# Optimization experiments

Hardware: AMD Instinct MI355X
Metric: run time of the kernel (lower is better)

The kernel has to match this reference:

```python
import jax, jax.numpy as jnp
from jax import lax
import numpy as np

B = 512
IN_CAPS, OUT_CAPS, IN_DIM, OUT_DIM, ITERS = 32 * 6 * 6, 10, 8, 16, 3
EPS = 1e-8


def setup_inputs() -> dict:
    key = jax.random.key(0)
    ks = jax.random.split(key, 12)
    inp = {
        "x": jax.random.normal(ks[0], (B, 1, 28, 28), dtype=jnp.float32),
        "conv1_w": jax.random.normal(ks[1], (256, 1, 9, 9), dtype=jnp.float32) * 0.05,
        "conv1_b": jnp.zeros((256,), dtype=jnp.float32),
        "conv2_w": jax.random.normal(ks[2], (256, 256, 9, 9), dtype=jnp.float32) * 0.02,
        "conv2_b": jnp.zeros((256,), dtype=jnp.float32),
        "W": jax.random.normal(ks[3], (IN_CAPS, OUT_CAPS, IN_DIM, OUT_DIM), dtype=jnp.float32) * 0.1,
        "d1_w": jax.random.normal(ks[4], (OUT_DIM * OUT_CAPS, 512), dtype=jnp.float32) * 0.05,
        "d1_b": jnp.zeros((512,), dtype=jnp.float32),
        "d2_w": jax.random.normal(ks[5], (512, 1024), dtype=jnp.float32) * 0.05,
        "d2_b": jnp.zeros((1024,), dtype=jnp.float32),
        "d3_w": jax.random.normal(ks[6], (1024, 28 * 28), dtype=jnp.float32) * 0.05,
        "d3_b": jnp.zeros((28 * 28,), dtype=jnp.float32),
    }
    return inp


def _squash(s):
    # s2/(1+s2) * s/sqrt(s2+eps), norm over last dim
    s2 = jnp.sum(s * s, axis=-1, keepdims=True)
    return s2 / (1.0 + s2) * (s / jnp.sqrt(s2 + EPS))


def _conv(x, w, b, stride):
    y = lax.conv_general_dilated(x, w, (stride, stride), "VALID",
                                 dimension_numbers=("NCHW", "OIHW", "NCHW"))
    return y + b[None, :, None, None]


def reference(x, conv1_w, conv1_b, conv2_w, conv2_b, W,
              d1_w, d1_b, d2_w, d2_b, d3_w, d3_b):
    h = jax.nn.relu(_conv(x, conv1_w, conv1_b, 1))          # [B,256,20,20]
    h = _conv(h, conv2_w, conv2_b, 2)                       # [B,256,6,6]
    u = h.reshape(h.shape[0], 8, IN_CAPS).transpose(0, 2, 1)  # [B,1152,8]
    u = _squash(u)

    # dynamic routing
    u_hat = jnp.einsum("ijnm,bin->bijm", W, u)              # [B,1152,10,16]
    b_log = jnp.zeros((u.shape[0], IN_CAPS, OUT_CAPS), dtype=u.dtype)
    v = None
    for _ in range(ITERS):
        c = jax.nn.softmax(b_log, axis=1)                   # over in_capsules (as original)
        s = jnp.einsum("bij,bijm->bjm", c, u_hat)           # [B,10,16]
        v = _squash(s)
        b_log = b_log + jnp.einsum("bjm,bijm->bij", v, u_hat)
    caps = v                                                # [B,10,16]

    pred = jnp.argmax(jnp.sum(caps * caps, axis=-1), axis=-1)  # [B]
    mask = jax.lax.stop_gradient(jax.nn.one_hot(pred, OUT_CAPS, dtype=caps.dtype))
    dec_in = (caps * mask[:, :, None]).reshape(caps.shape[0], -1)  # [B,160]
    r = jax.nn.relu(dec_in @ d1_w + d1_b)
    r = jax.nn.relu(r @ d2_w + d2_b)
    r = jax.nn.sigmoid(r @ d3_w + d3_b)
    recon = r.reshape(-1, 1, 28, 28)
    return caps, recon, pred
```

## Files before the change

kernel.cpp:

```cpp
#include <hip/hip_runtime.h>

#define CAPS_EPS 1e-8f

typedef __attribute__((ext_vector_type(8))) short short8;
typedef __attribute__((ext_vector_type(4))) float f32x4;

__device__ inline ushort bf16_rn(float f) {
    uint u = __float_as_uint(f);
    u += 0x7fff + ((u >> 16) & 1);
    return (ushort)(u >> 16);
}
__device__ inline float bf16_f(ushort h) { return __uint_as_float((uint)h << 16); }

__device__ __forceinline__ void gld16(const void* g, void* l) {
    __builtin_amdgcn_global_load_lds(
        (const __attribute__((address_space(1))) unsigned int*)g,
        (__attribute__((address_space(3))) unsigned int*)l, 16, 0, 0);
}


__global__ __launch_bounds__(256) void k_wt2(const float* __restrict__ w2,
                                             ushort* __restrict__ wBhi,
                                             ushort* __restrict__ wBlo) {
    int n = blockIdx.x;
    int c = threadIdx.x;
    const float* src = w2 + (size_t)n * 20736 + c * 81;
    ushort* dh = wBhi + (size_t)n * 20736 + c;
    ushort* dl = wBlo + (size_t)n * 20736 + c;
    for (int t = 0; t < 81; ++t) {
        float f = src[t];
        ushort hi = bf16_rn(f);
        ushort lo = bf16_rn(f - bf16_f(hi));
        dh[t * 256] = hi;
        dl[t * 256] = lo;
    }
}

__global__ __launch_bounds__(256) void k_conv1(const float* __restrict__ x,
                                               const float* __restrict__ w1,
                                               const float* __restrict__ b1,
                                               ushort* __restrict__ h1hi,
                                               ushort* __restrict__ h1lo) {
    int blk = blockIdx.x;
    int b = blk / 5, strip = blk % 5;
    int y0 = strip * 4;
    int c = threadIdx.x;
    float w[81];
#pragma unroll
    for (int k = 0; k < 81; ++k) w[k] = w1[c * 81 + k];
    float bias = b1[c];
    const float* xb = x + (size_t)b * 784;
    for (int dy = 0; dy < 4; ++dy) {
        int y = y0 + dy;
        float acc[20];
#pragma unroll
        for (int i = 0; i < 20; ++i) acc[i] = bias;
#pragma unroll
        for (int ky = 0; ky < 9; ++ky) {
            float xr[28];
            const float4* xp = reinterpret_cast<const float4*>(xb + (y + ky) * 28);
#pragma unroll
            for (int q = 0; q < 7; ++q) {
                float4 v = xp[q];
                xr[q * 4 + 0] = v.x; xr[q * 4 + 1] = v.y;
                xr[q * 4 + 2] = v.z; xr[q * 4 + 3] = v.w;
            }
#pragma unroll
            for (int kx = 0; kx < 9; ++kx) {
                float wv = w[ky * 9 + kx];
#pragma unroll
                for (int xo = 0; xo < 20; ++xo)
                    acc[xo] = fmaf(xr[xo + kx], wv, acc[xo]);
            }
        }
#pragma unroll
        for (int xo = 0; xo < 20; ++xo) {
            float a = fmaxf(acc[xo], 0.f);
            ushort hi = bf16_rn(a);
            ushort lo = bf16_rn(a - bf16_f(hi));
            size_t o = ((size_t)(b * 20 + y) * 20 + xo) * 256 + c;
            h1hi[o] = hi;
            h1lo[o] = lo;
        }
    }
}

__global__ __launch_bounds__(256) void k_h2init(const float* __restrict__ b2,
                                                float* __restrict__ h2) {
    h2[(size_t)blockIdx.x * 256 + threadIdx.x] = b2[threadIdx.x];
}

__global__ __launch_bounds__(256) void k_zero4(float* __restrict__ p) {
    reinterpret_cast<float4*>(p)[(size_t)blockIdx.x * 256 + threadIdx.x] = make_float4(0, 0, 0, 0);
}

__global__ __launch_bounds__(256, 2) void k_conv2m(const ushort* __restrict__ h1hi,
                                                   const ushort* __restrict__ h1lo,
                                                   const ushort* __restrict__ wBhi,
                                                   const ushort* __restrict__ wBlo,
                                                   float* __restrict__ h2) {
    __shared__ ushort Ahi[128 * 32];
    __shared__ ushort Alo[128 * 32];
    __shared__ ushort Bhi[256 * 32];
    __shared__ ushort Blo[256 * 32];
    int tid = threadIdx.x;
    int m0 = blockIdx.x * 128;
    int kbase = blockIdx.y * 2592;

    int wv = tid >> 6, lane = tid & 63;
    int cq = (lane & 3) * 8;

    int ra = wv * 32 + (lane >> 2);
    int mA0 = m0 + ra, mA1 = mA0 + 16;
    int mb0 = mA0 / 36, mp0 = mA0 - mb0 * 36;
    int mb1 = mA1 / 36, mp1 = mA1 - mb1 * 36;
    size_t a0 = ((size_t)mb0 * 400 + (mp0 / 6) * 40 + (mp0 % 6) * 2) * 256 + cq;
    size_t a1 = ((size_t)mb1 * 400 + (mp1 / 6) * 40 + (mp1 % 6) * 2) * 256 + cq;
    int ldsA = wv * 1024;

    int rb = wv * 64 + (lane >> 2);
    size_t bB = (size_t)rb * 20736 + cq;
    int ldsB = wv * 2048;

    int mhalf = (wv >> 1) * 64, nhalf = (wv & 1) * 128;
    int lrow = lane & 15, quad = lane >> 4;

    f32x4 acc[4][8];
#pragma unroll
    for (int a = 0; a < 4; ++a)
#pragma unroll
        for (int bq = 0; bq < 8; ++bq) acc[a][bq] = (f32x4){0.f, 0.f, 0.f, 0.f};

    for (int ks = 0; ks < 81; ++ks) {
        int k = kbase + ks * 32;
        int t = k >> 8, cc = k & 255;
        int ky = t / 9, kx = t - ky * 9;
        size_t koffA = (size_t)(ky * 5120 + kx * 256 + cc);

        __syncthreads();
        gld16(h1hi + a0 + koffA, &Ahi[ldsA]);
        gld16(h1hi + a1 + koffA, &Ahi[ldsA + 512]);
        gld16(h1lo + a0 + koffA, &Alo[ldsA]);
        gld16(h1lo + a1 + koffA, &Alo[ldsA + 512]);
#pragma unroll
        for (int q = 0; q < 4; ++q) {
            size_t bo = bB + (size_t)q * 331776 + k;
            gld16(wBhi + bo, &Bhi[ldsB + q * 512]);
            gld16(wBlo + bo, &Blo[ldsB + q * 512]);
        }
        __syncthreads();

        short8 ah[4], al[4];
#pragma unroll
        for (int tm = 0; tm < 4; ++tm) {
            int off = (mhalf + tm * 16 + lrow) * 32 + quad * 8;
            ah[tm] = *reinterpret_cast<short8*>(&Ahi[off]);
            al[tm] = *reinterpret_cast<short8*>(&Alo[off]);
        }
#pragma unroll
        for (int tn = 0; tn < 8; ++tn) {
            int off = (nhalf + tn * 16 + lrow) * 32 + quad * 8;
            short8 bh = *reinterpret_cast<short8*>(&Bhi[off]);
            short8 bl2 = *reinterpret_cast<short8*>(&Blo[off]);
#pragma unroll
            for (int tm = 0; tm < 4; ++tm) {
                acc[tm][tn] = __builtin_amdgcn_mfma_f32_16x16x32_bf16(ah[tm], bh, acc[tm][tn], 0, 0, 0);
                acc[tm][tn] = __builtin_amdgcn_mfma_f32_16x16x32_bf16(ah[tm], bl2, acc[tm][tn], 0, 0, 0);
                acc[tm][tn] = __builtin_amdgcn_mfma_f32_16x16x32_bf16(al[tm], bh, acc[tm][tn], 0, 0, 0);
            }
        }
    }

#pragma unroll
    for (int tm = 0; tm < 4; ++tm) {
        int mrow = m0 + mhalf + tm * 16 + quad * 4;
#pragma unroll
        for (int tn = 0; tn < 8; ++tn) {
            int ncol = nhalf + tn * 16 + lrow;
#pragma unroll
            for (int r = 0; r < 4; ++r)
                atomicAdd(&h2[(size_t)(mrow + r) * 256 + ncol], acc[tm][tn][r]);
        }
    }
}

__global__ __launch_bounds__(256) void k_squashT(const float* __restrict__ h2,
                                                 float* __restrict__ uT) {
    int i = blockIdx.x;
    int b = blockIdx.y * 256 + threadIdx.x;
    int g = i / 36, s = i - g * 36;
    const float* hp = h2 + ((size_t)b * 36 + s) * 256 + g;
    float val[8];
    float s2 = 0.f;
#pragma unroll
    for (int n = 0; n < 8; ++n) {
        val[n] = hp[n * 32];
        s2 = fmaf(val[n], val[n], s2);
    }
    float scale = s2 / ((1.f + s2) * sqrtf(s2 + CAPS_EPS));
#pragma unroll
    for (int n = 0; n < 8; ++n)
        uT[((size_t)i * 8 + n) * 512 + b] = val[n] * scale;
}

__global__ __launch_bounds__(256) void k_s(const float* __restrict__ Wc,
                                           const float* __restrict__ uT,
                                           const float* __restrict__ bl,
                                           const float* __restrict__ Z,
                                           float* __restrict__ sT,
                                           int first) {
    __shared__ float lw[8 * 1280];
    int tid = threadIdx.x;
    int i0 = blockIdx.x * 8;
    int b = blockIdx.y * 128 + (tid & 127);
    int mh = tid >> 7;
    const float* wg = Wc + (size_t)i0 * 1280;
#pragma unroll
    for (int r = 0; r < 10; ++r) {
        int q4 = (r * 256 + tid) * 4;
        *reinterpret_cast<float4*>(&lw[q4]) = *reinterpret_cast<const float4*>(wg + q4);
    }
    __syncthreads();
    float rzs[10];
    if (!first) {
#pragma unroll
        for (int j = 0; j < 10; ++j) rzs[j] = 1.0f / Z[j * 512 + b];
    }
    float acc[80];
#pragma unroll
    for (int q = 0; q < 80; ++q) acc[q] = 0.f;
    for (int di = 0; di < 8; ++di) {
        int i = i0 + di;
        float ur[8];
#pragma unroll
        for (int n = 0; n < 8; ++n) ur[n] = uT[((size_t)i * 8 + n) * 512 + b];
#pragma unroll
        for (int j = 0; j < 10; ++j) {
            float c;
            if (first) c = (1.0f / 1152.0f);
            else c = expf(bl[((size_t)i * 10 + j) * 512 + b]) * rzs[j];
            const float* wp = &lw[((di * 10 + j) * 8) * 16 + mh * 8];
#pragma unroll
            for (int mm = 0; mm < 8; ++mm) {
                float uh = 0.f;
#pragma unroll
                for (int n = 0; n < 8; ++n) uh = fmaf(wp[n * 16 + mm], ur[n], uh);
                acc[j * 8 + mm] = fmaf(c, uh, acc[j * 8 + mm]);
            }
        }
    }
#pragma unroll
    for (int j = 0; j < 10; ++j)
#pragma unroll
        for (int mm = 0; mm < 8; ++mm)
            atomicAdd(&sT[(j * 16 + mh * 8 + mm) * 512 + b], acc[j * 8 + mm]);
}

__global__ __launch_bounds__(256) void k_v(const float* __restrict__ sT,
                                           float* __restrict__ v,
                                           float* __restrict__ vT,
                                           float* __restrict__ sTz,
                                           float* __restrict__ Z) {
    int idx = blockIdx.x * 256 + threadIdx.x;
    int j = idx >> 9;
    int b = idx & 511;
    float sv[16];
    float s2 = 0.f;
#pragma unroll
    for (int m = 0; m < 16; ++m) {
        sv[m] = sT[(j * 16 + m) * 512 + b];
        s2 = fmaf(sv[m], sv[m], s2);
    }
    float scale = s2 / ((1.f + s2) * sqrtf(s2 + CAPS_EPS));
#pragma unroll
    for (int m = 0; m < 16; ++m) {
        float val = sv[m] * scale;
        v[(size_t)b * 160 + j * 16 + m] = val;
        vT[(j * 16 + m) * 512 + b] = val;
        sTz[(j * 16 + m) * 512 + b] = 0.f;
    }
    Z[idx] = 0.f;
}

__global__ __launch_bounds__(256) void k_bupd(const float* __restrict__ Wc,
                                              const float* __restrict__ uT,
                                              const float* __restrict__ vT,
                                              float* __restrict__ bl,
                                              float* __restrict__ Z) {
    __shared__ float lw[8 * 1280];
    int tid = threadIdx.x;
    int i0 = blockIdx.x * 8;
    int b = blockIdx.y * 128 + (tid & 127);
    int ih = tid >> 7;
    const float* wg = Wc + (size_t)i0 * 1280;
#pragma unroll
    for (int r = 0; r < 10; ++r) {
        int q4 = (r * 256 + tid) * 4;
        *reinterpret_cast<float4*>(&lw[q4]) = *reinterpret_cast<const float4*>(wg + q4);
    }
    __syncthreads();
    float ur[4][8];
#pragma unroll
    for (int ii = 0; ii < 4; ++ii) {
        int i = i0 + ih * 4 + ii;
#pragma unroll
        for (int n = 0; n < 8; ++n) ur[ii][n] = uT[((size_t)i * 8 + n) * 512 + b];
    }
    for (int j = 0; j < 10; ++j) {
        float vj[16];
#pragma unroll
        for (int m = 0; m < 16; ++m) vj[m] = vT[(j * 16 + m) * 512 + b];
        float zp = 0.f;
#pragma unroll
        for (int ii = 0; ii < 4; ++ii) {
            int di = ih * 4 + ii;
            const float* wp = &lw[((di * 10 + j) * 8) * 16];
            float t = 0.f;
#pragma unroll
            for (int n = 0; n < 8; ++n) {
                float wvv = 0.f;
#pragma unroll
                for (int m = 0; m < 16; ++m) wvv = fmaf(wp[n * 16 + m], vj[m], wvv);
                t = fmaf(ur[ii][n], wvv, t);
            }
            size_t idx = ((size_t)(i0 + di) * 10 + j) * 512 + b;
            float nb = bl[idx] + t;
            bl[idx] = nb;
            zp += expf(nb);
        }
        atomicAdd(&Z[j * 512 + b], zp);
    }
}

__global__ __launch_bounds__(256) void k_pred(const float* __restrict__ v,
                                              float* __restrict__ out,
                                              float* __restrict__ dec,
                                              int pred_off) {
    int b = blockIdx.x, t = threadIdx.x;
    __shared__ float sq[160];
    __shared__ float nrm[10];
    __shared__ int ip;
    float val = 0.f;
    if (t < 160) {
        val = v[(size_t)b * 160 + t];
        out[(size_t)b * 160 + t] = val;
        sq[t] = val * val;
    }
    __syncthreads();
    if (t < 10) {
        float s = 0.f;
#pragma unroll
        for (int k = 0; k < 16; ++k) s += sq[t * 16 + k];
        nrm[t] = s;
    }
    __syncthreads();
    if (t == 0) {
        float best = nrm[0];
        int bi = 0;
        for (int j = 1; j < 10; ++j)
            if (nrm[j] > best) { best = nrm[j]; bi = j; }
        ip = bi;
        out[(size_t)pred_off + b] = (float)bi;
    }
    __syncthreads();
    if (t < 160) dec[(size_t)b * 160 + t] = ((t >> 4) == ip) ? val : 0.f;
}

template <int ACT>
__global__ __launch_bounds__(256) void k_gemm(const float* __restrict__ A,
                                              const float* __restrict__ B,
                                              const float* __restrict__ bias,
                                              float* __restrict__ C,
                                              int M, int K, int N) {
    __shared__ float As[16 * 64];
    __shared__ float Bs[16 * 64];
    int tid = threadIdx.x;
    int m0 = blockIdx.y * 64, n0 = blockIdx.x * 64;
    int arow = tid >> 2, akq = (tid & 3) * 4;
    int brow = tid >> 4, bcol = (tid & 15) * 4;
    int ty = tid >> 4, tx = tid & 15;
    float acc[4][4];
#pragma unroll
    for (int r = 0; r < 4; ++r)
#pragma unroll
        for (int q = 0; q < 4; ++q) acc[r][q] = 0.f;
    for (int k0 = 0; k0 < K; k0 += 16) {
        float4 av = *reinterpret_cast<const float4*>(A + (size_t)(m0 + arow) * K + k0 + akq);
        float4 bv = make_float4(0, 0, 0, 0);
        if (n0 + bcol < N)
            bv = *reinterpret_cast<const float4*>(B + (size_t)(k0 + brow) * N + n0 + bcol);
        __syncthreads();
        As[(akq + 0) * 64 + arow] = av.x;
        As[(akq + 1) * 64 + arow] = av.y;
        As[(akq + 2) * 64 + arow] = av.z;
        As[(akq + 3) * 64 + arow] = av.w;
        *reinterpret_cast<float4*>(&Bs[brow * 64 + bcol]) = bv;
        __syncthreads();
#pragma unroll
        for (int kk = 0; kk < 16; ++kk) {
            float4 a4 = *reinterpret_cast<float4*>(&As[kk * 64 + ty * 4]);
            float4 b4 = *reinterpret_cast<float4*>(&Bs[kk * 64 + tx * 4]);
            float ar[4] = {a4.x, a4.y, a4.z, a4.w};
            float br[4] = {b4.x, b4.y, b4.z, b4.w};
#pragma unroll
            for (int r = 0; r < 4; ++r)
#pragma unroll
                for (int q = 0; q < 4; ++q)
                    acc[r][q] = fmaf(ar[r], br[q], acc[r][q]);
        }
    }
#pragma unroll
    for (int r = 0; r < 4; ++r) {
        int mm = m0 + ty * 4 + r;
#pragma unroll
        for (int q = 0; q < 4; ++q) {
            int nn = n0 + tx * 4 + q;
            if (nn < N) {
                float val = acc[r][q] + bias[nn];
                if (ACT == 0) val = fmaxf(val, 0.f);
                else val = 1.f / (1.f + expf(-val));
                C[(size_t)mm * N + nn] = val;
            }
        }
    }
}

extern "C" void kernel_launch(void* const* d_in, const int* in_sizes, int n_in,
                              void* d_out, int out_size, void* d_ws, size_t ws_size,
                              hipStream_t stream) {
    const float* x   = (const float*)d_in[0];
    const float* w1  = (const float*)d_in[1];
    const float* b1  = (const float*)d_in[2];
    const float* w2  = (const float*)d_in[3];
    const float* b2  = (const float*)d_in[4];
    const float* Wc  = (const float*)d_in[5];
    const float* d1w = (const float*)d_in[6];
    const float* d1b = (const float*)d_in[7];
    const float* d2w = (const float*)d_in[8];
    const float* d2b = (const float*)d_in[9];
    const float* d3w = (const float*)d_in[10];
    const float* d3b = (const float*)d_in[11];
    float* out = (float*)d_out;

    ushort* wBhi = (ushort*)d_ws;
    ushort* wBlo = wBhi + 5308416;
    ushort* h1hi = (ushort*)((char*)d_ws + 21233664);
    ushort* h1lo = h1hi + 52428800;
    float*  h2   = (float*)((char*)d_ws + 230948864);

    float* post = (float*)((char*)d_ws + 21233664);
    float* uT  = post + 4718592;
    float* bl  = post + 9437184;
    float* sT  = post + 15335424;
    float* Z   = post + 15417344;
    float* v   = post + 15422464;
    float* vT  = post + 15504384;
    float* dec = post + 15586304;
    float* r1  = post + 15668224;
    float* r2  = post + 15930368;

    int pred_off = out_size - 512;

    k_wt2<<<256, 256, 0, stream>>>(w2, wBhi, wBlo);
    k_conv1<<<2560, 256, 0, stream>>>(x, w1, b1, h1hi, h1lo);
    k_h2init<<<18432, 256, 0, stream>>>(b2, h2);
    k_conv2m<<<dim3(144, 8), 256, 0, stream>>>(h1hi, h1lo, wBhi, wBlo, h2);
    k_zero4<<<5845, 256, 0, stream>>>(bl);
    k_squashT<<<dim3(1152, 2), 256, 0, stream>>>(h2, uT);

    for (int it = 0; it < 3; ++it) {
        k_s<<<dim3(144, 4), 256, 0, stream>>>(Wc, uT, bl, Z, sT, it == 0 ? 1 : 0);
        k_v<<<20, 256, 0, stream>>>(sT, v, vT, sT, Z);
        if (it < 2) k_bupd<<<dim3(144, 4), 256, 0, stream>>>(Wc, uT, vT, bl, Z);
    }

    k_pred<<<512, 256, 0, stream>>>(v, out, dec, pred_off);
    k_gemm<0><<<dim3(8, 8), 256, 0, stream>>>(dec, d1w, d1b, r1, 512, 160, 512);
    k_gemm<0><<<dim3(16, 8), 256, 0, stream>>>(r1, d2w, d2b, r2, 512, 512, 1024);
    k_gemm<1><<<dim3(13, 8), 256, 0, stream>>>(r2, d3w, d3b, out + 81920, 512, 1024, 784);
}
```

Baseline: 1.419 ms.

## Pipeline conv2 GEMM loads, merge weight prep with bias init, tile squash transpose

The conv2 MFMA kernel now double-buffers the A tile and splits the B tile into two 128-column halves. The load of one half overlaps with the MFMA work on the other, hiding global-to-LDS latency. The weight-transpose kernel is split across three times as many blocks and merged with the h2 bias-init kernel, removing one launch. The squash/transpose kernel is rewritten to stage h2 rows in shared memory so that both reads and writes coalesce. This adds synchronisation complexity and a larger LDS footprint.

```diff
diff --git a/kernel.cpp b/kernel.cpp
--- a/kernel.cpp
+++ b/kernel.cpp
@@ -19,20 +19,29 @@
 }
 
 
-__global__ __launch_bounds__(256) void k_wt2(const float* __restrict__ w2,
+__global__ __launch_bounds__(256) void k_pre(const float* __restrict__ w2,
                                              ushort* __restrict__ wBhi,
-                                             ushort* __restrict__ wBlo) {
-    int n = blockIdx.x;
-    int c = threadIdx.x;
-    const float* src = w2 + (size_t)n * 20736 + c * 81;
-    ushort* dh = wBhi + (size_t)n * 20736 + c;
-    ushort* dl = wBlo + (size_t)n * 20736 + c;
-    for (int t = 0; t < 81; ++t) {
-        float f = src[t];
-        ushort hi = bf16_rn(f);
-        ushort lo = bf16_rn(f - bf16_f(hi));
-        dh[t * 256] = hi;
-        dl[t * 256] = lo;
+                                             ushort* __restrict__ wBlo,
+                                             const float* __restrict__ b2,
+                                             float* __restrict__ h2) {
+    int bx = blockIdx.x;
+    if (bx < 768) {
+        int n = bx & 255;
+        int t0 = (bx >> 8) * 27;
+        int c = threadIdx.x;
+        const float* src = w2 + (size_t)n * 20736 + c * 81;
+        ushort* dh = wBhi + (size_t)n * 20736 + c;
+        ushort* dl = wBlo + (size_t)n * 20736 + c;
+        for (int t = t0; t < t0 + 27; ++t) {
+            float f = src[t];
+            ushort hi = bf16_rn(f);
+            ushort lo = bf16_rn(f - bf16_f(hi));
+            dh[t * 256] = hi;
+            dl[t * 256] = lo;
+        }
+    } else {
+        int r = bx - 768;
+        h2[(size_t)r * 256 + threadIdx.x] = b2[threadIdx.x];
     }
 }
 
@@ -85,11 +94,6 @@
     }
 }
 
-__global__ __launch_bounds__(256) void k_h2init(const float* __restrict__ b2,
-                                                float* __restrict__ h2) {
-    h2[(size_t)blockIdx.x * 256 + threadIdx.x] = b2[threadIdx.x];
-}
-
 __global__ __launch_bounds__(256) void k_zero4(float* __restrict__ p) {
     reinterpret_cast<float4*>(p)[(size_t)blockIdx.x * 256 + threadIdx.x] = make_float4(0, 0, 0, 0);
 }
@@ -99,10 +103,10 @@
                                                    const ushort* __restrict__ wBhi,
                                                    const ushort* __restrict__ wBlo,
                                                    float* __restrict__ h2) {
-    __shared__ ushort Ahi[128 * 32];
-    __shared__ ushort Alo[128 * 32];
-    __shared__ ushort Bhi[256 * 32];
-    __shared__ ushort Blo[256 * 32];
+    __shared__ ushort Ah[2][4096];
+    __shared__ ushort Al[2][4096];
+    __shared__ ushort Bh[2][4096];
+    __shared__ ushort Bl[2][4096];
     int tid = threadIdx.x;
     int m0 = blockIdx.x * 128;
     int kbase = blockIdx.y * 2592;
@@ -118,11 +122,11 @@
     size_t a1 = ((size_t)mb1 * 400 + (mp1 / 6) * 40 + (mp1 % 6) * 2) * 256 + cq;
     int ldsA = wv * 1024;
 
-    int rb = wv * 64 + (lane >> 2);
+    int rb = wv * 32 + (lane >> 2);
     size_t bB = (size_t)rb * 20736 + cq;
-    int ldsB = wv * 2048;
-
-    int mhalf = (wv >> 1) * 64, nhalf = (wv & 1) * 128;
+    int ldsB = wv * 1024;
+
+    int mhalf = (wv >> 1) * 64, nq = (wv & 1) * 64;
     int lrow = lane & 15, quad = lane >> 4;
 
     f32x4 acc[4][8];
@@ -131,37 +135,46 @@
 #pragma unroll
         for (int bq = 0; bq < 8; ++bq) acc[a][bq] = (f32x4){0.f, 0.f, 0.f, 0.f};
 
+#define ISSUE_A(KS, Q)                                                     \
+    {                                                                      \
+        int k_ = kbase + (KS) * 32;                                        \
+        int t_ = k_ >> 8, cc_ = k_ & 255;                                  \
+        int ky_ = t_ / 9, kx_ = t_ - ky_ * 9;                              \
+        size_t ko_ = (size_t)(ky_ * 5120 + kx_ * 256 + cc_);               \
+        gld16(h1hi + a0 + ko_, &Ah[Q][ldsA]);                              \
+        gld16(h1hi + a1 + ko_, &Ah[Q][ldsA + 512]);                        \
+        gld16(h1lo + a0 + ko_, &Al[Q][ldsA]);                              \
+        gld16(h1lo + a1 + ko_, &Al[Q][ldsA + 512]);                        \
+    }
+#define ISSUE_B(KS, NH, P)                                                 \
+    {                                                                      \
+        size_t bo_ = bB + (size_t)(NH) * 2654208 + kbase + (KS) * 32;      \
+        gld16(wBhi + bo_, &Bh[P][ldsB]);                                   \
+        gld16(wBhi + bo_ + 331776, &Bh[P][ldsB + 512]);                    \
+        gld16(wBlo + bo_, &Bl[P][ldsB]);                                   \
+        gld16(wBlo + bo_ + 331776, &Bl[P][ldsB + 512]);                    \
+    }
+
+    ISSUE_A(0, 0);
+    ISSUE_B(0, 0, 0);
+
     for (int ks = 0; ks < 81; ++ks) {
-        int k = kbase + ks * 32;
-        int t = k >> 8, cc = k & 255;
-        int ky = t / 9, kx = t - ky * 9;
-        size_t koffA = (size_t)(ky * 5120 + kx * 256 + cc);
+        int q = ks & 1;
+        short8 ah[4], al[4];
 
         __syncthreads();
-        gld16(h1hi + a0 + koffA, &Ahi[ldsA]);
-        gld16(h1hi + a1 + koffA, &Ahi[ldsA + 512]);
-        gld16(h1lo + a0 + koffA, &Alo[ldsA]);
-        gld16(h1lo + a1 + koffA, &Alo[ldsA + 512]);
-#pragma unroll
-        for (int q = 0; q < 4; ++q) {
-            size_t bo = bB + (size_t)q * 331776 + k;
-            gld16(wBhi + bo, &Bhi[ldsB + q * 512]);
-            gld16(wBlo + bo, &Blo[ldsB + q * 512]);
-        }
-        __syncthreads();
-
-        short8 ah[4], al[4];
+        ISSUE_B(ks, 1, 1);
 #pragma unroll
         for (int tm = 0; tm < 4; ++tm) {
             int off = (mhalf + tm * 16 + lrow) * 32 + quad * 8;
-            ah[tm] = *reinterpret_cast<short8*>(&Ahi[off]);
-            al[tm] = *reinterpret_cast<short8*>(&Alo[off]);
-        }
-#pragma unroll
-        for (int tn = 0; tn < 8; ++tn) {
-            int off = (nhalf + tn * 16 + lrow) * 32 + quad * 8;
-            short8 bh = *reinterpret_cast<short8*>(&Bhi[off]);
-            short8 bl2 = *reinterpret_cast<short8*>(&Blo[off]);
+            ah[tm] = *reinterpret_cast<short8*>(&Ah[q][off]);
+            al[tm] = *reinterpret_cast<short8*>(&Al[q][off]);
+        }
+#pragma unroll
+        for (int tn = 0; tn < 4; ++tn) {
+            int off = (nq + tn * 16 + lrow) * 32 + quad * 8;
+            short8 bh = *reinterpret_cast<short8*>(&Bh[0][off]);
+            short8 bl2 = *reinterpret_cast<short8*>(&Bl[0][off]);
 #pragma unroll
             for (int tm = 0; tm < 4; ++tm) {
                 acc[tm][tn] = __builtin_amdgcn_mfma_f32_16x16x32_bf16(ah[tm], bh, acc[tm][tn], 0, 0, 0);
@@ -169,38 +182,70 @@
                 acc[tm][tn] = __builtin_amdgcn_mfma_f32_16x16x32_bf16(al[tm], bh, acc[tm][tn], 0, 0, 0);
             }
         }
-    }
+
+        __syncthreads();
+        if (ks < 80) {
+            ISSUE_A(ks + 1, q ^ 1);
+            ISSUE_B(ks + 1, 0, 0);
+        }
+#pragma unroll
+        for (int tn = 0; tn < 4; ++tn) {
+            int off = (nq + tn * 16 + lrow) * 32 + quad * 8;
+            short8 bh = *reinterpret_cast<short8*>(&Bh[1][off]);
+            short8 bl2 = *reinterpret_cast<short8*>(&Bl[1][off]);
+#pragma unroll
+            for (int tm = 0; tm < 4; ++tm) {
+                acc[tm][4 + tn] = __builtin_amdgcn_mfma_f32_16x16x32_bf16(ah[tm], bh, acc[tm][4 + tn], 0, 0, 0);
+                acc[tm][4 + tn] = __builtin_amdgcn_mfma_f32_16x16x32_bf16(ah[tm], bl2, acc[tm][4 + tn], 0, 0, 0);
+                acc[tm][4 + tn] = __builtin_amdgcn_mfma_f32_16x16x32_bf16(al[tm], bh, acc[tm][4 + tn], 0, 0, 0);
+            }
+        }
+    }
+#undef ISSUE_A
+#undef ISSUE_B
 
 #pragma unroll
     for (int tm = 0; tm < 4; ++tm) {
         int mrow = m0 + mhalf + tm * 16 + quad * 4;
 #pragma unroll
-        for (int tn = 0; tn < 8; ++tn) {
-            int ncol = nhalf + tn * 16 + lrow;
+        for (int j = 0; j < 8; ++j) {
+            int ncol = (j >> 2) * 128 + nq + (j & 3) * 16 + lrow;
 #pragma unroll
             for (int r = 0; r < 4; ++r)
-                atomicAdd(&h2[(size_t)(mrow + r) * 256 + ncol], acc[tm][tn][r]);
-        }
-    }
-}
-
-__global__ __launch_bounds__(256) void k_squashT(const float* __restrict__ h2,
-                                                 float* __restrict__ uT) {
-    int i = blockIdx.x;
-    int b = blockIdx.y * 256 + threadIdx.x;
-    int g = i / 36, s = i - g * 36;
-    const float* hp = h2 + ((size_t)b * 36 + s) * 256 + g;
-    float val[8];
-    float s2 = 0.f;
-#pragma unroll
-    for (int n = 0; n < 8; ++n) {
-        val[n] = hp[n * 32];
-        s2 = fmaf(val[n], val[n], s2);
-    }
-    float scale = s2 / ((1.f + s2) * sqrtf(s2 + CAPS_EPS));
-#pragma unroll
-    for (int n = 0; n < 8; ++n)
-        uT[((size_t)i * 8 + n) * 512 + b] = val[n] * scale;
+                atomicAdd(&h2[(size_t)(mrow + r) * 256 + ncol], acc[tm][j][r]);
+        }
+    }
+}
+
+__global__ __launch_bounds__(256) void k_squashT2(const float* __restrict__ h2,
+                                                  float* __restrict__ uT) {
+    __shared__ float ld[32][257];
+    __shared__ float scl[32][33];
+    int s = blockIdx.x;
+    int b0 = blockIdx.y * 32;
+    int t = threadIdx.x;
+    for (int bb = 0; bb < 32; ++bb)
+        ld[bb][t] = h2[((size_t)(b0 + bb) * 36 + s) * 256 + t];
+    __syncthreads();
+    int b = t & 31, gb = (t >> 5) * 4;
+#pragma unroll
+    for (int q = 0; q < 4; ++q) {
+        int g = gb + q;
+        float s2 = 0.f;
+#pragma unroll
+        for (int n = 0; n < 8; ++n) {
+            float vv = ld[b][g + n * 32];
+            s2 = fmaf(vv, vv, s2);
+        }
+        scl[b][g] = s2 / ((1.f + s2) * sqrtf(s2 + CAPS_EPS));
+    }
+    __syncthreads();
+    int hf = t >> 5;
+    for (int gg = 0; gg < 32; ++gg) {
+        int idx = hf * 32 + gg;
+        int g = idx >> 3, n = idx & 7;
+        uT[(((size_t)g * 36 + s) * 8 + n) * 512 + b0 + b] = ld[b][g + n * 32] * scl[b][g];
+    }
 }
 
 __global__ __launch_bounds__(256) void k_s(const float* __restrict__ Wc,
@@ -461,12 +506,11 @@
 
     int pred_off = out_size - 512;
 
-    k_wt2<<<256, 256, 0, stream>>>(w2, wBhi, wBlo);
+    k_pre<<<768 + 18432, 256, 0, stream>>>(w2, wBhi, wBlo, b2, h2);
     k_conv1<<<2560, 256, 0, stream>>>(x, w1, b1, h1hi, h1lo);
-    k_h2init<<<18432, 256, 0, stream>>>(b2, h2);
     k_conv2m<<<dim3(144, 8), 256, 0, stream>>>(h1hi, h1lo, wBhi, wBlo, h2);
     k_zero4<<<5845, 256, 0, stream>>>(bl);
-    k_squashT<<<dim3(1152, 2), 256, 0, stream>>>(h2, uT);
+    k_squashT2<<<dim3(36, 16), 256, 0, stream>>>(h2, uT);
 
     for (int it = 0; it < 3; ++it) {
         k_s<<<dim3(144, 4), 256, 0, stream>>>(Wc, uT, bl, Z, sT, it == 0 ? 1 : 0);
```

After: 1.435 ms. No clear change (+1.1%).

## Move conv1 to split-bf16 MFMA, coalesce weight transpose and squash, vectorise routing

Applied to the files above, without the earlier changes.

Conv1 now runs as an implicit GEMM on bf16 MFMA, using hi/lo split inputs and weights that a new fused preprocessing kernel produces. The same kernel transposes the conv2 weights through shared memory so global reads and writes coalesce. The squash/transpose kernel stages tiles in LDS to avoid strided global reads. The routing kernels read W with float4 LDS loads. Together these aim to cut scalar FMA and uncoalesced-memory costs, at the price of three-product bf16 split precision in conv1 and an extra input-conversion pass.

```diff
diff --git a/kernel.cpp b/kernel.cpp
--- a/kernel.cpp
+++ b/kernel.cpp
@@ -19,70 +19,130 @@
 }
 
 
-__global__ __launch_bounds__(256) void k_wt2(const float* __restrict__ w2,
+__global__ __launch_bounds__(256) void k_pre(const float* __restrict__ w2,
                                              ushort* __restrict__ wBhi,
-                                             ushort* __restrict__ wBlo) {
-    int n = blockIdx.x;
-    int c = threadIdx.x;
-    const float* src = w2 + (size_t)n * 20736 + c * 81;
-    ushort* dh = wBhi + (size_t)n * 20736 + c;
-    ushort* dl = wBlo + (size_t)n * 20736 + c;
-    for (int t = 0; t < 81; ++t) {
-        float f = src[t];
+                                             ushort* __restrict__ wBlo,
+                                             const float* __restrict__ x,
+                                             ushort* __restrict__ xhi,
+                                             ushort* __restrict__ xlo,
+                                             const float* __restrict__ w1,
+                                             ushort* __restrict__ w1phi,
+                                             ushort* __restrict__ w1plo) {
+    int bx = blockIdx.x, tid = threadIdx.x;
+    if (bx < 256) {
+        __shared__ float ld[81 * 65];
+        int n = bx;
+        const float* src = w2 + (size_t)n * 20736;
+        for (int cc = 0; cc < 4; ++cc) {
+            for (int i = tid; i < 5184; i += 256) {
+                int c_loc = i / 81, t = i - c_loc * 81;
+                ld[t * 65 + c_loc] = src[cc * 5184 + i];
+            }
+            __syncthreads();
+            for (int i = tid; i < 5184; i += 256) {
+                int t = i >> 6, c_loc = i & 63;
+                float f = ld[t * 65 + c_loc];
+                ushort hi = bf16_rn(f);
+                ushort lo = bf16_rn(f - bf16_f(hi));
+                size_t o = (size_t)n * 20736 + t * 256 + cc * 64 + c_loc;
+                wBhi[o] = hi;
+                wBlo[o] = lo;
+            }
+            __syncthreads();
+        }
+    } else if (bx < 256 + 1569) {
+        int idx = (bx - 256) * 256 + tid;
+        if (idx < 401408) {
+            float f = x[idx];
+            ushort hi = bf16_rn(f);
+            ushort lo = bf16_rn(f - bf16_f(hi));
+            xhi[idx] = hi;
+            xlo[idx] = lo;
+        } else if (idx < 401472) {
+            xhi[idx] = 0;
+            xlo[idx] = 0;
+        }
+    } else {
+        int idx = (bx - 1825) * 256 + tid;
+        int c = idx / 160;
+        int kk160 = idx - c * 160;
+        int kstep = kk160 >> 5, kk = kk160 & 31;
+        int ky = kstep * 2 + (kk >> 4), kx = kk & 15;
+        float f = (ky < 9 && kx < 9) ? w1[c * 81 + ky * 9 + kx] : 0.f;
         ushort hi = bf16_rn(f);
         ushort lo = bf16_rn(f - bf16_f(hi));
-        dh[t * 256] = hi;
-        dl[t * 256] = lo;
-    }
-}
-
-__global__ __launch_bounds__(256) void k_conv1(const float* __restrict__ x,
-                                               const float* __restrict__ w1,
-                                               const float* __restrict__ b1,
-                                               ushort* __restrict__ h1hi,
-                                               ushort* __restrict__ h1lo) {
-    int blk = blockIdx.x;
-    int b = blk / 5, strip = blk % 5;
-    int y0 = strip * 4;
-    int c = threadIdx.x;
-    float w[81];
-#pragma unroll
-    for (int k = 0; k < 81; ++k) w[k] = w1[c * 81 + k];
-    float bias = b1[c];
-    const float* xb = x + (size_t)b * 784;
-    for (int dy = 0; dy < 4; ++dy) {
-        int y = y0 + dy;
-        float acc[20];
-#pragma unroll
-        for (int i = 0; i < 20; ++i) acc[i] = bias;
-#pragma unroll
-        for (int ky = 0; ky < 9; ++ky) {
-            float xr[28];
-            const float4* xp = reinterpret_cast<const float4*>(xb + (y + ky) * 28);
-#pragma unroll
-            for (int q = 0; q < 7; ++q) {
-                float4 v = xp[q];
-                xr[q * 4 + 0] = v.x; xr[q * 4 + 1] = v.y;
-                xr[q * 4 + 2] = v.z; xr[q * 4 + 3] = v.w;
-            }
-#pragma unroll
-            for (int kx = 0; kx < 9; ++kx) {
-                float wv = w[ky * 9 + kx];
-#pragma unroll
-                for (int xo = 0; xo < 20; ++xo)
-                    acc[xo] = fmaf(xr[xo + kx], wv, acc[xo]);
-            }
-        }
-#pragma unroll
-        for (int xo = 0; xo < 20; ++xo) {
-            float a = fmaxf(acc[xo], 0.f);
-            ushort hi = bf16_rn(a);
-            ushort lo = bf16_rn(a - bf16_f(hi));
-            size_t o = ((size_t)(b * 20 + y) * 20 + xo) * 256 + c;
-            h1hi[o] = hi;
-            h1lo[o] = lo;
-        }
-    }
+        w1phi[idx] = hi;
+        w1plo[idx] = lo;
+    }
+}
+
+__global__ __launch_bounds__(256) void k_conv1m(const ushort* __restrict__ xhi,
+                                                const ushort* __restrict__ xlo,
+                                                const ushort* __restrict__ w1phi,
+                                                const ushort* __restrict__ w1plo,
+                                                const float* __restrict__ b1,
+                                                ushort* __restrict__ h1hi,
+                                                ushort* __restrict__ h1lo) {
+    int tid = threadIdx.x;
+    int wv = tid >> 6, lane = tid & 63;
+    int lrow = lane & 15, quad = lane >> 4;
+    int m0 = blockIdx.x * 128 + wv * 32;
+    int c0 = blockIdx.y * 64;
+
+    int am[2];
+#pragma unroll
+    for (int t = 0; t < 2; ++t) {
+        int m = m0 + t * 16 + lrow;
+        int b = m / 400, r = m - b * 400;
+        int y = r / 20, xx = r - y * 20;
+        am[t] = b * 784 + y * 28 + xx;
+    }
+
+    f32x4 acc[2][4];
+#pragma unroll
+    for (int t = 0; t < 2; ++t)
+#pragma unroll
+        for (int tn = 0; tn < 4; ++tn) acc[t][tn] = (f32x4){0.f, 0.f, 0.f, 0.f};
+
+    for (int kstep = 0; kstep < 5; ++kstep) {
+        int arow = (kstep * 2 + (quad >> 1)) * 28 + (quad & 1) * 8;
+        int boff = kstep * 32 + quad * 8;
+        short8 bh[4], bl2[4];
+#pragma unroll
+        for (int tn = 0; tn < 4; ++tn) {
+            int br = (c0 + tn * 16 + lrow) * 160 + boff;
+            bh[tn] = *reinterpret_cast<const short8*>(w1phi + br);
+            bl2[tn] = *reinterpret_cast<const short8*>(w1plo + br);
+        }
+#pragma unroll
+        for (int t = 0; t < 2; ++t) {
+            short8 ah = *reinterpret_cast<const short8*>(xhi + am[t] + arow);
+            short8 al = *reinterpret_cast<const short8*>(xlo + am[t] + arow);
+#pragma unroll
+            for (int tn = 0; tn < 4; ++tn) {
+                acc[t][tn] = __builtin_amdgcn_mfma_f32_16x16x32_bf16(ah, bh[tn], acc[t][tn], 0, 0, 0);
+                acc[t][tn] = __builtin_amdgcn_mfma_f32_16x16x32_bf16(ah, bl2[tn], acc[t][tn], 0, 0, 0);
+                acc[t][tn] = __builtin_amdgcn_mfma_f32_16x16x32_bf16(al, bh[tn], acc[t][tn], 0, 0, 0);
+            }
+        }
+    }
+
+#pragma unroll
+    for (int t = 0; t < 2; ++t)
+#pragma unroll
+        for (int r = 0; r < 4; ++r) {
+            int m = m0 + t * 16 + quad * 4 + r;
+#pragma unroll
+            for (int tn = 0; tn < 4; ++tn) {
+                int c = c0 + tn * 16 + lrow;
+                float v = acc[t][tn][r] + b1[c];
+                v = fmaxf(v, 0.f);
+                ushort hi = bf16_rn(v);
+                ushort lo = bf16_rn(v - bf16_f(hi));
+                h1hi[(size_t)m * 256 + c] = hi;
+                h1lo[(size_t)m * 256 + c] = lo;
+            }
+        }
 }
 
 __global__ __launch_bounds__(256) void k_h2init(const float* __restrict__ b2,
@@ -184,23 +244,35 @@
     }
 }
 
-__global__ __launch_bounds__(256) void k_squashT(const float* __restrict__ h2,
-                                                 float* __restrict__ uT) {
-    int i = blockIdx.x;
-    int b = blockIdx.y * 256 + threadIdx.x;
-    int g = i / 36, s = i - g * 36;
-    const float* hp = h2 + ((size_t)b * 36 + s) * 256 + g;
-    float val[8];
-    float s2 = 0.f;
-#pragma unroll
-    for (int n = 0; n < 8; ++n) {
-        val[n] = hp[n * 32];
-        s2 = fmaf(val[n], val[n], s2);
-    }
-    float scale = s2 / ((1.f + s2) * sqrtf(s2 + CAPS_EPS));
-#pragma unroll
-    for (int n = 0; n < 8; ++n)
-        uT[((size_t)i * 8 + n) * 512 + b] = val[n] * scale;
+__global__ __launch_bounds__(256) void k_squashT2(const float* __restrict__ h2,
+                                                  float* __restrict__ uT) {
+    __shared__ float ld[32][257];
+    __shared__ float scl[32][33];
+    int s = blockIdx.x;
+    int b0 = blockIdx.y * 32;
+    int t = threadIdx.x;
+    for (int bb = 0; bb < 32; ++bb)
+        ld[bb][t] = h2[((size_t)(b0 + bb) * 36 + s) * 256 + t];
+    __syncthreads();
+    int b = t & 31, gb = (t >> 5) * 4;
+#pragma unroll
+    for (int q = 0; q < 4; ++q) {
+        int g = gb + q;
+        float s2 = 0.f;
+#pragma unroll
+        for (int n = 0; n < 8; ++n) {
+            float vv = ld[b][g + n * 32];
+            s2 = fmaf(vv, vv, s2);
+        }
+        scl[b][g] = s2 / ((1.f + s2) * sqrtf(s2 + CAPS_EPS));
+    }
+    __syncthreads();
+    int hf = t >> 5;
+    for (int gg = 0; gg < 32; ++gg) {
+        int idx = hf * 32 + gg;
+        int g = idx >> 3, n = idx & 7;
+        uT[(((size_t)g * 36 + s) * 8 + n) * 512 + b0 + b] = ld[b][g + n * 32] * scl[b][g];
+    }
 }
 
 __global__ __launch_bounds__(256) void k_s(const float* __restrict__ Wc,
@@ -239,14 +311,26 @@
             float c;
             if (first) c = (1.0f / 1152.0f);
             else c = expf(bl[((size_t)i * 10 + j) * 512 + b]) * rzs[j];
-            const float* wp = &lw[((di * 10 + j) * 8) * 16 + mh * 8];
-#pragma unroll
-            for (int mm = 0; mm < 8; ++mm) {
-                float uh = 0.f;
-#pragma unroll
-                for (int n = 0; n < 8; ++n) uh = fmaf(wp[n * 16 + mm], ur[n], uh);
-                acc[j * 8 + mm] = fmaf(c, uh, acc[j * 8 + mm]);
-            }
+            const float* wp = &lw[(di * 10 + j) * 128 + mh * 8];
+            float4 s0 = {0.f, 0.f, 0.f, 0.f}, s1 = {0.f, 0.f, 0.f, 0.f};
+#pragma unroll
+            for (int n = 0; n < 8; ++n) {
+                const float4* wq = reinterpret_cast<const float4*>(wp + n * 16);
+                float4 wa = wq[0], wb = wq[1];
+                float un = ur[n];
+                s0.x = fmaf(un, wa.x, s0.x); s0.y = fmaf(un, wa.y, s0.y);
+                s0.z = fmaf(un, wa.z, s0.z); s0.w = fmaf(un, wa.w, s0.w);
+                s1.x = fmaf(un, wb.x, s1.x); s1.y = fmaf(un, wb.y, s1.y);
+                s1.z = fmaf(un, wb.z, s1.z); s1.w = fmaf(un, wb.w, s1.w);
+            }
+            acc[j * 8 + 0] = fmaf(c, s0.x, acc[j * 8 + 0]);
+            acc[j * 8 + 1] = fmaf(c, s0.y, acc[j * 8 + 1]);
+            acc[j * 8 + 2] = fmaf(c, s0.z, acc[j * 8 + 2]);
+            acc[j * 8 + 3] = fmaf(c, s0.w, acc[j * 8 + 3]);
+            acc[j * 8 + 4] = fmaf(c, s1.x, acc[j * 8 + 4]);
+            acc[j * 8 + 5] = fmaf(c, s1.y, acc[j * 8 + 5]);
+            acc[j * 8 + 6] = fmaf(c, s1.z, acc[j * 8 + 6]);
+            acc[j * 8 + 7] = fmaf(c, s1.w, acc[j * 8 + 7]);
         }
     }
 #pragma unroll
@@ -314,13 +398,21 @@
 #pragma unroll
         for (int ii = 0; ii < 4; ++ii) {
             int di = ih * 4 + ii;
-            const float* wp = &lw[((di * 10 + j) * 8) * 16];
+            const float* wp = &lw[(di * 10 + j) * 128];
             float t = 0.f;
 #pragma unroll
             for (int n = 0; n < 8; ++n) {
-                float wvv = 0.f;
-#pragma unroll
-                for (int m = 0; m < 16; ++m) wvv = fmaf(wp[n * 16 + m], vj[m], wvv);
+                const float4* wq = reinterpret_cast<const float4*>(wp + n * 16);
+                float4 w0 = wq[0], w1 = wq[1], w2 = wq[2], w3 = wq[3];
+                float wvv = w0.x * vj[0];
+                wvv = fmaf(w0.y, vj[1], wvv);  wvv = fmaf(w0.z, vj[2], wvv);
+                wvv = fmaf(w0.w, vj[3], wvv);  wvv = fmaf(w1.x, vj[4], wvv);
+                wvv = fmaf(w1.y, vj[5], wvv);  wvv = fmaf(w1.z, vj[6], wvv);
+                wvv = fmaf(w1.w, vj[7], wvv);  wvv = fmaf(w2.x, vj[8], wvv);
+                wvv = fmaf(w2.y, vj[9], wvv);  wvv = fmaf(w2.z, vj[10], wvv);
+                wvv = fmaf(w2.w, vj[11], wvv); wvv = fmaf(w3.x, vj[12], wvv);
+                wvv = fmaf(w3.y, vj[13], wvv); wvv = fmaf(w3.z, vj[14], wvv);
+                wvv = fmaf(w3.w, vj[15], wvv);
                 t = fmaf(ur[ii][n], wvv, t);
             }
             size_t idx = ((size_t)(i0 + di) * 10 + j) * 512 + b;
@@ -446,7 +538,12 @@
     ushort* wBlo = wBhi + 5308416;
     ushort* h1hi = (ushort*)((char*)d_ws + 21233664);
     ushort* h1lo = h1hi + 52428800;
-    float*  h2   = (float*)((char*)d_ws + 230948864);
+    char*   h2b  = (char*)d_ws + 230948864;
+    float*  h2   = (float*)h2b;
+    ushort* xhi   = (ushort*)h2b;
+    ushort* xlo   = xhi + 401472;
+    ushort* w1phi = xlo + 401472;
+    ushort* w1plo = w1phi + 40960;
 
     float* post = (float*)((char*)d_ws + 21233664);
     float* uT  = post + 4718592;
@@ -461,12 +558,12 @@
 
     int pred_off = out_size - 512;
 
-    k_wt2<<<256, 256, 0, stream>>>(w2, wBhi, wBlo);
-    k_conv1<<<2560, 256, 0, stream>>>(x, w1, b1, h1hi, h1lo);
+    k_pre<<<1985, 256, 0, stream>>>(w2, wBhi, wBlo, x, xhi, xlo, w1, w1phi, w1plo);
+    k_conv1m<<<dim3(1600, 4), 256, 0, stream>>>(xhi, xlo, w1phi, w1plo, b1, h1hi, h1lo);
     k_h2init<<<18432, 256, 0, stream>>>(b2, h2);
     k_conv2m<<<dim3(144, 8), 256, 0, stream>>>(h1hi, h1lo, wBhi, wBlo, h2);
     k_zero4<<<5845, 256, 0, stream>>>(bl);
-    k_squashT<<<dim3(1152, 2), 256, 0, stream>>>(h2, uT);
+    k_squashT2<<<dim3(36, 16), 256, 0, stream>>>(h2, uT);
 
     for (int it = 0; it < 3; ++it) {
         k_s<<<dim3(144, 4), 256, 0, stream>>>(Wc, uT, bl, Z, sT, it == 0 ? 1 : 0);
```

Result: faster. 1.373 ms (-3.3%).
